# Performance work log

Hardware: AMD Instinct MI355X
Metric: run time of the kernel (lower is better)

## Reference

```python
import jax, jax.numpy as jnp
import numpy as np

H = 2048       # hidden_size
F = 1024       # moe_intermediate_size
E = 32         # n_routed_experts
G = 8          # n_group
TOPK_GROUP = 3
TOP_K = 6      # num_experts_per_tok
N_SHARED = 2
SCALE = 1.0    # routed_scaling_factor
B, S = 1, 2048


def setup_inputs() -> dict:
    key = jax.random.key(0)
    ks = jax.random.split(key, 8)
    std = 0.02
    return {
        "hidden_states": jax.random.normal(ks[0], (B, S, H), dtype=jnp.float32),
        "w_gate": jax.random.normal(ks[1], (E, H), dtype=jnp.float32) * std,
        "wg": jax.random.normal(ks[2], (E, H, F), dtype=jnp.float32) * std,  # stacked gate_proj
        "wu": jax.random.normal(ks[3], (E, H, F), dtype=jnp.float32) * std,  # stacked up_proj
        "wd": jax.random.normal(ks[4], (E, F, H), dtype=jnp.float32) * std,  # stacked down_proj
        "sg": jax.random.normal(ks[5], (N_SHARED * F, H), dtype=jnp.float32) * std,  # shared gate_proj
        "su": jax.random.normal(ks[6], (N_SHARED * F, H), dtype=jnp.float32) * std,  # shared up_proj
        "sd": jax.random.normal(ks[7], (H, N_SHARED * F), dtype=jnp.float32) * std,  # shared down_proj
    }


def reference(hidden_states, w_gate, wg, wu, wd, sg, su, sd):
    b, s, h = hidden_states.shape
    x = hidden_states.reshape(-1, h)                    # [T, H]
    T = x.shape[0]

    # ---- MoEGate (softmax scoring, group_limited_greedy top-k) ----
    logits = x.astype(jnp.float32) @ w_gate.T           # [T, E]
    scores = jax.nn.softmax(logits, axis=-1)
    group_scores = scores.reshape(T, G, E // G).max(axis=-1)          # [T, G]
    _, group_idx = jax.lax.top_k(group_scores, TOPK_GROUP)            # [T, topk_group]
    group_mask = jax.nn.one_hot(group_idx, G, dtype=scores.dtype).sum(axis=1)  # [T, G]
    score_mask = jnp.repeat(group_mask, E // G, axis=-1)              # [T, E]
    tmp_scores = jnp.where(score_mask > 0.5, scores, 0.0)
    topk_weight, topk_idx = jax.lax.top_k(tmp_scores, TOP_K)          # [T, K]
    # norm_topk_prob=True, top_k>1
    topk_weight = topk_weight / (topk_weight.sum(axis=-1, keepdims=True) + 1e-20) * SCALE

    # combine weights per (token, expert): scatter topk weights (indices distinct)
    combine_w = jnp.zeros((T, E), dtype=jnp.float32)
    combine_w = combine_w.at[jnp.arange(T)[:, None], topk_idx].add(topk_weight)

    # ---- routed experts: dense grouped GEMMs, weighted combine ----
    g = jnp.einsum('th,ehf->etf', x, wg)                # [E, T, F]
    u = jnp.einsum('th,ehf->etf', x, wu)                # [E, T, F]
    act = jax.nn.silu(g) * u                            # SiLU gated
    act = act * combine_w.T[:, :, None]                 # fold combine weights before down-proj
    y = jnp.einsum('etf,efh->th', act, wd)              # [T, H]

    # ---- shared experts ----
    shared = (jax.nn.silu(x @ sg.T) * (x @ su.T)) @ sd.T

    return (y + shared).reshape(b, s, h)
```

## Files before the change

### kernel.cpp

```cpp
#include <hip/hip_runtime.h>

#define HD   2048
#define FD   1024
#define NEXP 32
#define TOPK 6
#define TT   2048
#define SDIM 2048
#define NPAIR (TT*TOPK)

typedef __bf16 bf16x8 __attribute__((ext_vector_type(8)));
typedef float  f32x4  __attribute__((ext_vector_type(4)));

#define GLOAD_LDS16(g, l) __builtin_amdgcn_global_load_lds( \
    (const __attribute__((address_space(1))) void*)(g),     \
    (__attribute__((address_space(3))) void*)(l), 16, 0, 0)

#define WAIT_VM4  asm volatile("s_waitcnt vmcnt(4)" ::: "memory")
#define WAIT_VM3  asm volatile("s_waitcnt vmcnt(3)" ::: "memory")
#define WAIT_VM0  asm volatile("s_waitcnt vmcnt(0)" ::: "memory")
#define BAR() do { __builtin_amdgcn_s_barrier(); } while (0)

__device__ __forceinline__ ushort f2b(float f) {
  __bf16 h = (__bf16)f;
  union { __bf16 h; ushort u; } v; v.h = h;
  return v.u;
}

__device__ __forceinline__ int xcd_swz(int bid, int nact) {
  int xcd = bid & 7, i = bid >> 3;
  int q = nact >> 3, r = nact & 7;
  int base = (xcd < r) ? xcd * (q + 1) : r * (q + 1) + (xcd - r) * q;
  return base + i;
}

__device__ __forceinline__ void argmax32(float &v, int &i) {
  #pragma unroll
  for (int m = 16; m >= 1; m >>= 1) {
    float ov = __shfl_xor(v, m, 32);
    int   oi = __shfl_xor(i, m, 32);
    if (ov > v || (ov == v && oi < i)) { v = ov; i = oi; }
  }
}

__global__ __launch_bounds__(64) void gating_kernel(
    const float* __restrict__ x, const float* __restrict__ wgate,
    int* __restrict__ topk_idx, float* __restrict__ topk_w, int* __restrict__ cnt)
{
  int t = blockIdx.x;
  int l = threadIdx.x;
  int e = l & 31;
  int half = l >> 5;
  const float* xr = x + (size_t)t * HD + half * (HD/2);
  const float* wr = wgate + (size_t)e * HD + half * (HD/2);
  float acc = 0.f;
  for (int i = 0; i < HD/2; i += 4) {
    float4 a = *(const float4*)(xr + i);
    float4 b = *(const float4*)(wr + i);
    acc += a.x*b.x + a.y*b.y + a.z*b.z + a.w*b.w;
  }
  acc += __shfl_xor(acc, 32);
  float logit = acc;
  float mx = logit;
  #pragma unroll
  for (int m = 16; m >= 1; m >>= 1) mx = fmaxf(mx, __shfl_xor(mx, m, 32));
  float p = __expf(logit - mx);
  float s = p;
  #pragma unroll
  for (int m = 16; m >= 1; m >>= 1) s += __shfl_xor(s, m, 32);
  float score = p / s;
  float gs = score;
  gs = fmaxf(gs, __shfl_xor(gs, 1, 32));
  gs = fmaxf(gs, __shfl_xor(gs, 2, 32));
  int g = e >> 2;
  float gw = gs;
  bool ingroup = false;
  for (int r = 0; r < 3; ++r) {
    float v = gw; int gi = g;
    argmax32(v, gi);
    if (g == gi) { ingroup = true; gw = -1.f; }
  }
  float ms = ingroup ? score : 0.f;
  int myrank = -1;
  float denom = 1e-20f;
  float mw = ms;
  for (int r = 0; r < 6; ++r) {
    float v = mw; int ei = e;
    argmax32(v, ei);
    denom += v;
    if (e == ei) { myrank = r; mw = -1.f; }
  }
  if (l < 32 && myrank >= 0) {
    topk_idx[t*TOPK + myrank] = e;
    topk_w  [t*TOPK + myrank] = score / denom;
    atomicAdd(&cnt[e], 1);
  }
}

__global__ void scan_kernel(const int* __restrict__ cnt, int* __restrict__ offs,
                            int* __restrict__ tl_e, int* __restrict__ tl_m, int* __restrict__ ntl) {
  if (threadIdx.x == 0) {
    int o = 0, nt = 0;
    for (int e = 0; e < NEXP; ++e) {
      offs[e] = o;
      for (int m = 0; m < cnt[e]; m += 256) { tl_e[nt] = e; tl_m[nt] = m; ++nt; }
      o += cnt[e];
    }
    ntl[0] = nt;
  }
}

__global__ void fill_kernel(const int* __restrict__ topk_idx, const float* __restrict__ topk_w,
                            const int* __restrict__ offs, int* __restrict__ cur,
                            int* __restrict__ pair_tok, float* __restrict__ pair_w)
{
  int idx = blockIdx.x * blockDim.x + threadIdx.x;
  if (idx >= NPAIR) return;
  int e = topk_idx[idx];
  int p = offs[e] + atomicAdd(&cur[e], 1);
  pair_tok[p] = idx / TOPK;
  pair_w[p]   = topk_w[idx];
}

__global__ void cvt_kernel(const float* __restrict__ x, ushort* __restrict__ xb) {
  int i = blockIdx.x * blockDim.x + threadIdx.x;
  float4 v = ((const float4*)x)[i];
  ((ushort4*)xb)[i] = make_ushort4(f2b(v.x), f2b(v.y), f2b(v.z), f2b(v.w));
}

__global__ __launch_bounds__(256) void fconv(const float* __restrict__ in, ushort* __restrict__ out) {
  int i = blockIdx.x * blockDim.x + threadIdx.x;
  float4 v = ((const float4*)in)[i];
  ((ushort4*)out)[i] = make_ushort4(f2b(v.x), f2b(v.y), f2b(v.z), f2b(v.w));
}

#define TSTR 76
__global__ __launch_bounds__(256) void tconv(const float* __restrict__ in, ushort* __restrict__ out,
                                             int R, int C) {
  __shared__ ushort T[64*TSTR];
  int tiles_c = C >> 6;
  int bt = blockIdx.x;
  int r0 = (bt / tiles_c) << 6;
  int c0 = (bt % tiles_c) << 6;
  const float* src = in + (size_t)blockIdx.y * R * C;
  ushort* dst = out + (size_t)blockIdx.y * R * C;
  int t = threadIdx.x;
  int row = (t >> 4) << 2;
  int col4 = (t & 15) << 2;
  float vv[4][4];
  #pragma unroll
  for (int i = 0; i < 4; ++i) {
    float4 v = *(const float4*)(src + (size_t)(r0 + row + i) * C + c0 + col4);
    vv[i][0] = v.x; vv[i][1] = v.y; vv[i][2] = v.z; vv[i][3] = v.w;
  }
  #pragma unroll
  for (int cc = 0; cc < 4; ++cc)
    *(ushort4*)&T[(col4 + cc)*TSTR + row] =
      make_ushort4(f2b(vv[0][cc]), f2b(vv[1][cc]), f2b(vv[2][cc]), f2b(vv[3][cc]));
  __syncthreads();
  #pragma unroll
  for (int p = 0; p < 2; ++p) {
    int item = t + p*256;
    int oc = item >> 3, seg = item & 7;
    ushort4 a = *(const ushort4*)&T[oc*TSTR + seg*8];
    ushort4 b = *(const ushort4*)&T[oc*TSTR + seg*8 + 4];
    ushort* d = dst + (size_t)(c0 + oc) * R + r0 + seg*8;
    *(ushort4*)(d)     = a;
    *(ushort4*)(d + 4) = b;
  }
}


__global__ __launch_bounds__(512, 4) void gu_routed_b(
    const ushort* __restrict__ xb, const ushort* __restrict__ wgt, const ushort* __restrict__ wut,
    const int* __restrict__ pair_tok, const float* __restrict__ pair_w,
    const int* __restrict__ cnt, const int* __restrict__ offs,
    const int* __restrict__ tl_e, const int* __restrict__ tl_m, const int* __restrict__ ntl,
    ushort* __restrict__ act)
{
  __shared__ ushort A[3][256*32];
  __shared__ ushort Bg[3][64*32];
  __shared__ ushort Bu[3][64*32];

  int nact = ntl[0] * 16;
  int bid = blockIdx.x;
  if (bid >= nact) return;
  int wid = xcd_swz(bid, nact);
  int tile = wid >> 4;
  int nt = wid & 15;
  int e  = tl_e[tile];
  int m0 = tl_m[tile];
  int ce = cnt[e];
  int oe = offs[e];
  int n0 = nt * 64;
  int tid = threadIdx.x, lane = tid & 63, w = tid >> 6;

  int csrc = (lane & 3) ^ ((lane >> 3) & 3);
  const ushort* asrc[2];
  #pragma unroll
  for (int j = 0; j < 2; ++j) {
    int r = (2*w + j)*16 + (lane >> 2);
    int pi = min(m0 + r, ce - 1);
    asrc[j] = xb + (size_t)pair_tok[oe + pi] * HD + csrc * 8;
  }
  int tsel = w >> 2;
  int bw = w & 3;
  const ushort* bsrc = (tsel ? wut : wgt) +
      ((size_t)e * FD + n0 + bw*16 + (lane >> 2)) * HD + csrc * 8;
  ushort* bdst0 = tsel ? &Bu[0][bw*512] : &Bg[0][bw*512];
  ushort* bdst1 = tsel ? &Bu[1][bw*512] : &Bg[1][bw*512];
  ushort* bdst2 = tsel ? &Bu[2][bw*512] : &Bg[2][bw*512];

  int lm = lane & 15, lg = lane >> 4;
  int wr = w >> 1, wc = w & 1;
  int asw = (lm >> 1) & 3;

  f32x4 accg[4][2], accu[4][2];
  #pragma unroll
  for (int m = 0; m < 4; ++m)
    #pragma unroll
    for (int n = 0; n < 2; ++n) { accg[m][n] = f32x4{0,0,0,0}; accu[m][n] = f32x4{0,0,0,0}; }

  #define GUB_ISSUE(T, BUF, BD) do { \
    GLOAD_LDS16(asrc[0] + (T)*32, &A[BUF][(2*w)*512]); \
    GLOAD_LDS16(asrc[1] + (T)*32, &A[BUF][(2*w+1)*512]); \
    GLOAD_LDS16(bsrc + (T)*32, BD); \
  } while (0)
  #define GUB_COMPUTE(BUF) do { \
    bf16x8 a[4], bg[2], bu[2]; \
    _Pragma("unroll") \
    for (int m = 0; m < 4; ++m) \
      a[m] = *(const bf16x8*)&A[BUF][(wr*64 + m*16 + lm)*32 + (lg ^ asw)*8]; \
    _Pragma("unroll") \
    for (int n = 0; n < 2; ++n) { \
      int row = wc*32 + n*16 + lm; \
      bg[n] = *(const bf16x8*)&Bg[BUF][row*32 + (lg ^ asw)*8]; \
      bu[n] = *(const bf16x8*)&Bu[BUF][row*32 + (lg ^ asw)*8]; \
    } \
    _Pragma("unroll") \
    for (int m = 0; m < 4; ++m) \
      _Pragma("unroll") \
      for (int n = 0; n < 2; ++n) { \
        accg[m][n] = __builtin_amdgcn_mfma_f32_16x16x32_bf16(a[m], bg[n], accg[m][n], 0, 0, 0); \
        accu[m][n] = __builtin_amdgcn_mfma_f32_16x16x32_bf16(a[m], bu[n], accu[m][n], 0, 0, 0); \
      } \
  } while (0)

  GUB_ISSUE(0, 0, bdst0);
  GUB_ISSUE(1, 1, bdst1);
  WAIT_VM3;
  BAR();

  for (int tt = 0; tt < 20; ++tt) {
    int t = tt * 3;
    GUB_ISSUE(t+2, 2, bdst2); GUB_COMPUTE(0); WAIT_VM3; BAR();
    GUB_ISSUE(t+3, 0, bdst0); GUB_COMPUTE(1); WAIT_VM3; BAR();
    GUB_ISSUE(t+4, 1, bdst1); GUB_COMPUTE(2); WAIT_VM3; BAR();
  }
  GUB_ISSUE(62, 2, bdst2); GUB_COMPUTE(0); WAIT_VM3; BAR();
  GUB_ISSUE(63, 0, bdst0); GUB_COMPUTE(1); WAIT_VM3; BAR();
  GUB_COMPUTE(2); WAIT_VM0; BAR();
  GUB_COMPUTE(0);
  #undef GUB_ISSUE
  #undef GUB_COMPUTE

  #pragma unroll
  for (int m = 0; m < 4; ++m) {
    #pragma unroll
    for (int j = 0; j < 4; ++j) {
      int rl = wr*64 + m*16 + lg*4 + j;
      int pi = m0 + rl;
      if (pi >= ce) continue;
      float pwv = pair_w[oe + pi];
      size_t base = (size_t)(oe + pi) * FD + n0 + wc*32;
      #pragma unroll
      for (int n = 0; n < 2; ++n) {
        float gv = accg[m][n][j];
        float uv = accu[m][n][j];
        float sv = gv / (1.f + __expf(-gv));
        act[base + n*16 + lm] = f2b(sv * uv * pwv);
      }
    }
  }
}

__global__ __launch_bounds__(512, 4) void down_routed_b(
    const ushort* __restrict__ act, const ushort* __restrict__ wdt,
    const int* __restrict__ pair_tok, const int* __restrict__ cnt, const int* __restrict__ offs,
    const int* __restrict__ tl_e, const int* __restrict__ tl_m, const int* __restrict__ ntl,
    float* __restrict__ y)
{
  __shared__ ushort A[3][256*32];
  __shared__ ushort Bd[3][128*32];

  int nact = ntl[0] * 16;
  int bid = blockIdx.x;
  if (bid >= nact) return;
  int wid = xcd_swz(bid, nact);
  int tile = wid >> 4;
  int nt = wid & 15;
  int e  = tl_e[tile];
  int m0 = tl_m[tile];
  int ce = cnt[e];
  int oe = offs[e];
  int n0 = nt * 128;
  int tid = threadIdx.x, lane = tid & 63, w = tid >> 6;

  int csrc = (lane & 3) ^ ((lane >> 3) & 3);
  const ushort* asrc[2];
  #pragma unroll
  for (int j = 0; j < 2; ++j) {
    int r = (2*w + j)*16 + (lane >> 2);
    int pi = min(m0 + r, ce - 1);
    asrc[j] = act + (size_t)(oe + pi) * FD + csrc * 8;
  }
  const ushort* bsrc = wdt + ((size_t)e * HD + n0 + w*16 + (lane >> 2)) * FD + csrc * 8;

  int lm = lane & 15, lg = lane >> 4;
  int wr = w >> 1, wc = w & 1;
  int asw = (lm >> 1) & 3;

  f32x4 acc[4][4];
  #pragma unroll
  for (int m = 0; m < 4; ++m)
    #pragma unroll
    for (int n = 0; n < 4; ++n) acc[m][n] = f32x4{0,0,0,0};

  #define DNB_ISSUE(T, BUF) do { \
    GLOAD_LDS16(asrc[0] + (T)*32, &A[BUF][(2*w)*512]); \
    GLOAD_LDS16(asrc[1] + (T)*32, &A[BUF][(2*w+1)*512]); \
    GLOAD_LDS16(bsrc + (T)*32, &Bd[BUF][w*512]); \
  } while (0)
  #define DNB_COMPUTE(BUF) do { \
    bf16x8 a[4], b[4]; \
    _Pragma("unroll") \
    for (int m = 0; m < 4; ++m) \
      a[m] = *(const bf16x8*)&A[BUF][(wr*64 + m*16 + lm)*32 + (lg ^ asw)*8]; \
    _Pragma("unroll") \
    for (int n = 0; n < 4; ++n) { \
      int row = wc*64 + n*16 + lm; \
      b[n] = *(const bf16x8*)&Bd[BUF][row*32 + (lg ^ asw)*8]; \
    } \
    _Pragma("unroll") \
    for (int m = 0; m < 4; ++m) \
      _Pragma("unroll") \
      for (int n = 0; n < 4; ++n) \
        acc[m][n] = __builtin_amdgcn_mfma_f32_16x16x32_bf16(a[m], b[n], acc[m][n], 0, 0, 0); \
  } while (0)

  DNB_ISSUE(0, 0);
  DNB_ISSUE(1, 1);
  WAIT_VM3;
  BAR();

  for (int tt = 0; tt < 10; ++tt) {
    int t = tt * 3;
    DNB_ISSUE(t+2, 2); DNB_COMPUTE(0); WAIT_VM3; BAR();
    DNB_ISSUE(t+3, 0); DNB_COMPUTE(1); WAIT_VM3; BAR();
    DNB_ISSUE(t+4, 1); DNB_COMPUTE(2); WAIT_VM3; BAR();
  }
  DNB_COMPUTE(0); WAIT_VM0; BAR();
  DNB_COMPUTE(1);
  #undef DNB_ISSUE
  #undef DNB_COMPUTE

  #pragma unroll
  for (int m = 0; m < 4; ++m) {
    #pragma unroll
    for (int j = 0; j < 4; ++j) {
      int rl = wr*64 + m*16 + lg*4 + j;
      int pi = m0 + rl;
      if (pi >= ce) continue;
      int tok = pair_tok[oe + pi];
      size_t base = (size_t)tok * HD + n0 + wc*64;
      #pragma unroll
      for (int n = 0; n < 4; ++n)
        atomicAdd(&y[base + n*16 + lm], acc[m][n][j]);
    }
  }
}

__global__ __launch_bounds__(256) void shared_gu_b(
    const ushort* __restrict__ xb, const ushort* __restrict__ sgb, const ushort* __restrict__ sub,
    ushort* __restrict__ sact)
{
  __shared__ ushort A[3][128*32];
  __shared__ ushort Bg[3][64*32];
  __shared__ ushort Bu[3][64*32];

  int bid = blockIdx.x;
  int wid = (bid & 7) * 64 + (bid >> 3);
  int mt = wid & 15;
  int nt = wid >> 4;
  int m0 = mt * 128;
  int n0 = nt * 64;
  int tid = threadIdx.x, lane = tid & 63, w = tid >> 6;

  int csrc = (lane & 3) ^ ((lane >> 3) & 3);
  const ushort* asrc[2];
  #pragma unroll
  for (int j = 0; j < 2; ++j) {
    int r = (2*w + j)*16 + (lane >> 2);
    asrc[j] = xb + (size_t)(m0 + r) * HD + csrc * 8;
  }
  int brow = w*16 + (lane >> 2);
  const ushort* bgsrc = sgb + (size_t)(n0 + brow) * HD + csrc * 8;
  const ushort* busrc = sub + (size_t)(n0 + brow) * HD + csrc * 8;

  int lm = lane & 15, lg = lane >> 4;
  int wr = w >> 1, wc = w & 1;
  int asw = (lm >> 1) & 3;

  f32x4 accg[4][2], accu[4][2];
  #pragma unroll
  for (int m = 0; m < 4; ++m)
    #pragma unroll
    for (int n = 0; n < 2; ++n) { accg[m][n] = f32x4{0,0,0,0}; accu[m][n] = f32x4{0,0,0,0}; }

  #define SGB_ISSUE(T, BUF) do { \
    GLOAD_LDS16(asrc[0] + (T)*32, &A[BUF][(2*w)*512]); \
    GLOAD_LDS16(asrc[1] + (T)*32, &A[BUF][(2*w+1)*512]); \
    GLOAD_LDS16(bgsrc + (T)*32, &Bg[BUF][w*512]); \
    GLOAD_LDS16(busrc + (T)*32, &Bu[BUF][w*512]); \
  } while (0)
  #define SGB_COMPUTE(BUF) do { \
    bf16x8 a[4], bg[2], bu[2]; \
    _Pragma("unroll") \
    for (int m = 0; m < 4; ++m) \
      a[m] = *(const bf16x8*)&A[BUF][(wr*64 + m*16 + lm)*32 + (lg ^ asw)*8]; \
    _Pragma("unroll") \
    for (int n = 0; n < 2; ++n) { \
      int row = wc*32 + n*16 + lm; \
      bg[n] = *(const bf16x8*)&Bg[BUF][row*32 + (lg ^ asw)*8]; \
      bu[n] = *(const bf16x8*)&Bu[BUF][row*32 + (lg ^ asw)*8]; \
    } \
    _Pragma("unroll") \
    for (int m = 0; m < 4; ++m) \
      _Pragma("unroll") \
      for (int n = 0; n < 2; ++n) { \
        accg[m][n] = __builtin_amdgcn_mfma_f32_16x16x32_bf16(a[m], bg[n], accg[m][n], 0, 0, 0); \
        accu[m][n] = __builtin_amdgcn_mfma_f32_16x16x32_bf16(a[m], bu[n], accu[m][n], 0, 0, 0); \
      } \
  } while (0)

  SGB_ISSUE(0, 0);
  SGB_ISSUE(1, 1);
  WAIT_VM4;
  BAR();

  for (int tt = 0; tt < 20; ++tt) {
    int t = tt * 3;
    SGB_ISSUE(t+2, 2); SGB_COMPUTE(0); WAIT_VM4; BAR();
    SGB_ISSUE(t+3, 0); SGB_COMPUTE(1); WAIT_VM4; BAR();
    SGB_ISSUE(t+4, 1); SGB_COMPUTE(2); WAIT_VM4; BAR();
  }
  SGB_ISSUE(62, 2); SGB_COMPUTE(0); WAIT_VM4; BAR();
  SGB_ISSUE(63, 0); SGB_COMPUTE(1); WAIT_VM4; BAR();
  SGB_COMPUTE(2); WAIT_VM0; BAR();
  SGB_COMPUTE(0);
  #undef SGB_ISSUE
  #undef SGB_COMPUTE

  #pragma unroll
  for (int m = 0; m < 4; ++m) {
    #pragma unroll
    for (int j = 0; j < 4; ++j) {
      int rl = wr*64 + m*16 + lg*4 + j;
      size_t base = (size_t)(m0 + rl) * SDIM + n0 + wc*32;
      #pragma unroll
      for (int n = 0; n < 2; ++n) {
        float gv = accg[m][n][j];
        float uv = accu[m][n][j];
        float sv = gv / (1.f + __expf(-gv));
        sact[base + n*16 + lm] = f2b(sv * uv);
      }
    }
  }
}

__global__ __launch_bounds__(256) void shared_down_b(
    const ushort* __restrict__ sact, const ushort* __restrict__ sdb, float* __restrict__ y)
{
  __shared__ ushort A[3][128*32];
  __shared__ ushort Bd[3][128*32];

  int bid = blockIdx.x;
  int wid = (bid & 7) * 32 + (bid >> 3);
  int mt = wid & 15;
  int nt = wid >> 4;
  int m0 = mt * 128;
  int n0 = nt * 128;
  int tid = threadIdx.x, lane = tid & 63, w = tid >> 6;

  int csrc = (lane & 3) ^ ((lane >> 3) & 3);
  const ushort* asrc[2];
  const ushort* bsrc[2];
  #pragma unroll
  for (int j = 0; j < 2; ++j) {
    int r = (2*w + j)*16 + (lane >> 2);
    asrc[j] = sact + (size_t)(m0 + r) * SDIM + csrc * 8;
    bsrc[j] = sdb + (size_t)(n0 + r) * SDIM + csrc * 8;
  }

  int lm = lane & 15, lg = lane >> 4;
  int wr = w >> 1, wc = w & 1;
  int asw = (lm >> 1) & 3;

  f32x4 acc[4][4];
  #pragma unroll
  for (int m = 0; m < 4; ++m)
    #pragma unroll
    for (int n = 0; n < 4; ++n) acc[m][n] = f32x4{0,0,0,0};

  #define SDB_ISSUE(T, BUF) do { \
    GLOAD_LDS16(asrc[0] + (T)*32, &A[BUF][(2*w)*512]); \
    GLOAD_LDS16(asrc[1] + (T)*32, &A[BUF][(2*w+1)*512]); \
    GLOAD_LDS16(bsrc[0] + (T)*32, &Bd[BUF][(2*w)*512]); \
    GLOAD_LDS16(bsrc[1] + (T)*32, &Bd[BUF][(2*w+1)*512]); \
  } while (0)
  #define SDB_COMPUTE(BUF) do { \
    bf16x8 a[4], b[4]; \
    _Pragma("unroll") \
    for (int m = 0; m < 4; ++m) \
      a[m] = *(const bf16x8*)&A[BUF][(wr*64 + m*16 + lm)*32 + (lg ^ asw)*8]; \
    _Pragma("unroll") \
    for (int n = 0; n < 4; ++n) { \
      int row = wc*64 + n*16 + lm; \
      b[n] = *(const bf16x8*)&Bd[BUF][row*32 + (lg ^ asw)*8]; \
    } \
    _Pragma("unroll") \
    for (int m = 0; m < 4; ++m) \
      _Pragma("unroll") \
      for (int n = 0; n < 4; ++n) \
        acc[m][n] = __builtin_amdgcn_mfma_f32_16x16x32_bf16(a[m], b[n], acc[m][n], 0, 0, 0); \
  } while (0)

  SDB_ISSUE(0, 0);
  SDB_ISSUE(1, 1);
  WAIT_VM4;
  BAR();

  for (int tt = 0; tt < 20; ++tt) {
    int t = tt * 3;
    SDB_ISSUE(t+2, 2); SDB_COMPUTE(0); WAIT_VM4; BAR();
    SDB_ISSUE(t+3, 0); SDB_COMPUTE(1); WAIT_VM4; BAR();
    SDB_ISSUE(t+4, 1); SDB_COMPUTE(2); WAIT_VM4; BAR();
  }
  SDB_ISSUE(62, 2); SDB_COMPUTE(0); WAIT_VM4; BAR();
  SDB_ISSUE(63, 0); SDB_COMPUTE(1); WAIT_VM4; BAR();
  SDB_COMPUTE(2); WAIT_VM0; BAR();
  SDB_COMPUTE(0);
  #undef SDB_ISSUE
  #undef SDB_COMPUTE

  #pragma unroll
  for (int m = 0; m < 4; ++m) {
    #pragma unroll
    for (int j = 0; j < 4; ++j) {
      int rl = wr*64 + m*16 + lg*4 + j;
      size_t base = (size_t)(m0 + rl) * HD + n0 + wc*64;
      #pragma unroll
      for (int n = 0; n < 4; ++n)
        y[base + n*16 + lm] = acc[m][n][j];
    }
  }
}

extern "C" void kernel_launch(void* const* d_in, const int* in_sizes, int n_in,
                              void* d_out, int out_size, void* d_ws, size_t ws_size,
                              hipStream_t stream) {
  const float* x     = (const float*)d_in[0];
  const float* wgate = (const float*)d_in[1];
  const float* wg    = (const float*)d_in[2];
  const float* wu    = (const float*)d_in[3];
  const float* wd    = (const float*)d_in[4];
  const float* sg    = (const float*)d_in[5];
  const float* su    = (const float*)d_in[6];
  const float* sd    = (const float*)d_in[7];
  float* y = (float*)d_out;
  char* ws = (char*)d_ws;

  ushort* xb   = (ushort*)(ws + 0);
  ushort* act  = (ushort*)(ws + 8388608);
  ushort* sact = (ushort*)(ws + 33554432);
  int*    tidx = (int*)  (ws + 41943040);
  float*  tw   = (float*)(ws + 41992192);
  int*    ptok = (int*)  (ws + 42041344);
  float*  pw   = (float*)(ws + 42090496);
  int*    cnt  = (int*)  (ws + 42139648);
  int*    curc = (int*)  (ws + 42139776);
  int*    offs = (int*)  (ws + 42139904);
  int*    tl_e = (int*)  (ws + 42140160);
  int*    tl_m = (int*)  (ws + 42140672);
  int*    ntl  = (int*)  (ws + 42141184);
  ushort* wgt  = (ushort*)(ws + 50331648);
  ushort* wut  = (ushort*)(ws + 184549376);
  ushort* wdt  = (ushort*)(ws + 318767104);
  ushort* sgb  = (ushort*)(ws + 452984832);
  ushort* sub  = (ushort*)(ws + 461373440);
  ushort* sdb  = (ushort*)(ws + 469762048);

  hipMemsetAsync(cnt, 0, 512, stream);

  cvt_kernel<<<dim3(4096), dim3(256), 0, stream>>>(x, xb);
  gating_kernel<<<dim3(TT), dim3(64), 0, stream>>>(x, wgate, tidx, tw, cnt);
  scan_kernel<<<dim3(1), dim3(64), 0, stream>>>(cnt, offs, tl_e, tl_m, ntl);
  fill_kernel<<<dim3(48), dim3(256), 0, stream>>>(tidx, tw, offs, curc, ptok, pw);

  tconv<<<dim3(512, NEXP), dim3(256), 0, stream>>>(wg, wgt, HD, FD);
  tconv<<<dim3(512, NEXP), dim3(256), 0, stream>>>(wu, wut, HD, FD);
  tconv<<<dim3(512, NEXP), dim3(256), 0, stream>>>(wd, wdt, FD, HD);
  fconv<<<dim3(4096), dim3(256), 0, stream>>>(sg, sgb);
  fconv<<<dim3(4096), dim3(256), 0, stream>>>(su, sub);
  fconv<<<dim3(4096), dim3(256), 0, stream>>>(sd, sdb);

  shared_gu_b<<<dim3(512), dim3(256), 0, stream>>>(xb, sgb, sub, sact);
  shared_down_b<<<dim3(256), dim3(256), 0, stream>>>(sact, sdb, y);
  gu_routed_b<<<dim3(1280), dim3(512), 0, stream>>>(xb, wgt, wut, ptok, pw, cnt, offs,
                                                    tl_e, tl_m, ntl, act);
  down_routed_b<<<dim3(1280), dim3(512), 0, stream>>>(act, wdt, ptok, cnt, offs,
                                                      tl_e, tl_m, ntl, y);
}
```

Before: 753.3 us.

## Replace routed down-proj atomics with per-pair bf16 output and gather combine; enlarge shared-expert tiles

The routed down-projection now writes each (token, expert) pair's result as bf16 into a pair-ordered buffer instead of doing float atomicAdds into y. A new combine kernel gathers the six pair rows per token through an inverse index built in fill_kernel and adds them to y. The shared-expert kernels move to 512-thread blocks with 256-row M tiles and fewer B-loads per thread. This removes atomic contention but adds a separate combine pass and rounds the pair partial sums to bf16, which could affect accuracy. The pair buffer reuses the transposed gate-weight workspace, which is safe only because gu_routed_b has already finished reading it.

```diff
diff --git a/kernel.cpp b/kernel.cpp
--- a/kernel.cpp
+++ b/kernel.cpp
@@ -15,7 +15,6 @@
     (const __attribute__((address_space(1))) void*)(g),     \
     (__attribute__((address_space(3))) void*)(l), 16, 0, 0)
 
-#define WAIT_VM4  asm volatile("s_waitcnt vmcnt(4)" ::: "memory")
 #define WAIT_VM3  asm volatile("s_waitcnt vmcnt(3)" ::: "memory")
 #define WAIT_VM0  asm volatile("s_waitcnt vmcnt(0)" ::: "memory")
 #define BAR() do { __builtin_amdgcn_s_barrier(); } while (0)
@@ -24,6 +23,10 @@
   __bf16 h = (__bf16)f;
   union { __bf16 h; ushort u; } v; v.h = h;
   return v.u;
+}
+__device__ __forceinline__ float b2f(ushort u) {
+  union { unsigned u; float f; } v; v.u = (unsigned)u << 16;
+  return v.f;
 }
 
 __device__ __forceinline__ int xcd_swz(int bid, int nact) {
@@ -111,7 +114,8 @@
 
 __global__ void fill_kernel(const int* __restrict__ topk_idx, const float* __restrict__ topk_w,
                             const int* __restrict__ offs, int* __restrict__ cur,
-                            int* __restrict__ pair_tok, float* __restrict__ pair_w)
+                            int* __restrict__ pair_tok, float* __restrict__ pair_w,
+                            int* __restrict__ inv)
 {
   int idx = blockIdx.x * blockDim.x + threadIdx.x;
   if (idx >= NPAIR) return;
@@ -119,6 +123,7 @@
   int p = offs[e] + atomicAdd(&cur[e], 1);
   pair_tok[p] = idx / TOPK;
   pair_w[p]   = topk_w[idx];
+  inv[idx]    = p;
 }
 
 __global__ void cvt_kernel(const float* __restrict__ x, ushort* __restrict__ xb) {
@@ -169,6 +174,29 @@
   }
 }
 
+__global__ __launch_bounds__(256) void combine_kernel(
+    const ushort* __restrict__ pairout, const int* __restrict__ inv, float* __restrict__ y)
+{
+  int t = blockIdx.x;
+  int h0 = threadIdx.x * 8;
+  const int* iv = inv + t*TOPK;
+  float* yr = y + (size_t)t * HD + h0;
+  float4 y0 = *(const float4*)(yr);
+  float4 y1 = *(const float4*)(yr + 4);
+  float acc[8] = {y0.x, y0.y, y0.z, y0.w, y1.x, y1.y, y1.z, y1.w};
+  #pragma unroll
+  for (int r = 0; r < TOPK; ++r) {
+    int p = iv[r];
+    const ushort* pr = pairout + (size_t)p * HD + h0;
+    ushort4 a = *(const ushort4*)(pr);
+    ushort4 b = *(const ushort4*)(pr + 4);
+    acc[0] += b2f(a.x); acc[1] += b2f(a.y); acc[2] += b2f(a.z); acc[3] += b2f(a.w);
+    acc[4] += b2f(b.x); acc[5] += b2f(b.y); acc[6] += b2f(b.z); acc[7] += b2f(b.w);
+  }
+  *(float4*)(yr)     = make_float4(acc[0], acc[1], acc[2], acc[3]);
+  *(float4*)(yr + 4) = make_float4(acc[4], acc[5], acc[6], acc[7]);
+}
+
 
 __global__ __launch_bounds__(512, 4) void gu_routed_b(
     const ushort* __restrict__ xb, const ushort* __restrict__ wgt, const ushort* __restrict__ wut,
@@ -285,9 +313,9 @@
 
 __global__ __launch_bounds__(512, 4) void down_routed_b(
     const ushort* __restrict__ act, const ushort* __restrict__ wdt,
-    const int* __restrict__ pair_tok, const int* __restrict__ cnt, const int* __restrict__ offs,
+    const int* __restrict__ cnt, const int* __restrict__ offs,
     const int* __restrict__ tl_e, const int* __restrict__ tl_m, const int* __restrict__ ntl,
-    float* __restrict__ y)
+    ushort* __restrict__ pairout)
 {
   __shared__ ushort A[3][256*32];
   __shared__ ushort Bd[3][128*32];
@@ -370,28 +398,27 @@
       int rl = wr*64 + m*16 + lg*4 + j;
       int pi = m0 + rl;
       if (pi >= ce) continue;
-      int tok = pair_tok[oe + pi];
-      size_t base = (size_t)tok * HD + n0 + wc*64;
+      size_t base = (size_t)(oe + pi) * HD + n0 + wc*64;
       #pragma unroll
       for (int n = 0; n < 4; ++n)
-        atomicAdd(&y[base + n*16 + lm], acc[m][n][j]);
+        pairout[base + n*16 + lm] = f2b(acc[m][n][j]);
     }
   }
 }
 
-__global__ __launch_bounds__(256) void shared_gu_b(
+__global__ __launch_bounds__(512, 4) void shared_gu_b(
     const ushort* __restrict__ xb, const ushort* __restrict__ sgb, const ushort* __restrict__ sub,
     ushort* __restrict__ sact)
 {
-  __shared__ ushort A[3][128*32];
+  __shared__ ushort A[3][256*32];
   __shared__ ushort Bg[3][64*32];
   __shared__ ushort Bu[3][64*32];
 
   int bid = blockIdx.x;
-  int wid = (bid & 7) * 64 + (bid >> 3);
-  int mt = wid & 15;
-  int nt = wid >> 4;
-  int m0 = mt * 128;
+  int wid = (bid & 7) * 32 + (bid >> 3);
+  int mt = wid & 7;
+  int nt = wid >> 3;
+  int m0 = mt * 256;
   int n0 = nt * 64;
   int tid = threadIdx.x, lane = tid & 63, w = tid >> 6;
 
@@ -402,9 +429,12 @@
     int r = (2*w + j)*16 + (lane >> 2);
     asrc[j] = xb + (size_t)(m0 + r) * HD + csrc * 8;
   }
-  int brow = w*16 + (lane >> 2);
-  const ushort* bgsrc = sgb + (size_t)(n0 + brow) * HD + csrc * 8;
-  const ushort* busrc = sub + (size_t)(n0 + brow) * HD + csrc * 8;
+  int tsel = w >> 2;
+  int bw = w & 3;
+  const ushort* bsrc = (tsel ? sub : sgb) + (size_t)(n0 + bw*16 + (lane >> 2)) * HD + csrc * 8;
+  ushort* bdst0 = tsel ? &Bu[0][bw*512] : &Bg[0][bw*512];
+  ushort* bdst1 = tsel ? &Bu[1][bw*512] : &Bg[1][bw*512];
+  ushort* bdst2 = tsel ? &Bu[2][bw*512] : &Bg[2][bw*512];
 
   int lm = lane & 15, lg = lane >> 4;
   int wr = w >> 1, wc = w & 1;
@@ -416,11 +446,10 @@
     #pragma unroll
     for (int n = 0; n < 2; ++n) { accg[m][n] = f32x4{0,0,0,0}; accu[m][n] = f32x4{0,0,0,0}; }
 
-  #define SGB_ISSUE(T, BUF) do { \
+  #define SGB_ISSUE(T, BUF, BD) do { \
     GLOAD_LDS16(asrc[0] + (T)*32, &A[BUF][(2*w)*512]); \
     GLOAD_LDS16(asrc[1] + (T)*32, &A[BUF][(2*w+1)*512]); \
-    GLOAD_LDS16(bgsrc + (T)*32, &Bg[BUF][w*512]); \
-    GLOAD_LDS16(busrc + (T)*32, &Bu[BUF][w*512]); \
+    GLOAD_LDS16(bsrc + (T)*32, BD); \
   } while (0)
   #define SGB_COMPUTE(BUF) do { \
     bf16x8 a[4], bg[2], bu[2]; \
@@ -442,19 +471,19 @@
       } \
   } while (0)
 
-  SGB_ISSUE(0, 0);
-  SGB_ISSUE(1, 1);
-  WAIT_VM4;
+  SGB_ISSUE(0, 0, bdst0);
+  SGB_ISSUE(1, 1, bdst1);
+  WAIT_VM3;
   BAR();
 
   for (int tt = 0; tt < 20; ++tt) {
     int t = tt * 3;
-    SGB_ISSUE(t+2, 2); SGB_COMPUTE(0); WAIT_VM4; BAR();
-    SGB_ISSUE(t+3, 0); SGB_COMPUTE(1); WAIT_VM4; BAR();
-    SGB_ISSUE(t+4, 1); SGB_COMPUTE(2); WAIT_VM4; BAR();
-  }
-  SGB_ISSUE(62, 2); SGB_COMPUTE(0); WAIT_VM4; BAR();
-  SGB_ISSUE(63, 0); SGB_COMPUTE(1); WAIT_VM4; BAR();
+    SGB_ISSUE(t+2, 2, bdst2); SGB_COMPUTE(0); WAIT_VM3; BAR();
+    SGB_ISSUE(t+3, 0, bdst0); SGB_COMPUTE(1); WAIT_VM3; BAR();
+    SGB_ISSUE(t+4, 1, bdst1); SGB_COMPUTE(2); WAIT_VM3; BAR();
+  }
+  SGB_ISSUE(62, 2, bdst2); SGB_COMPUTE(0); WAIT_VM3; BAR();
+  SGB_ISSUE(63, 0, bdst0); SGB_COMPUTE(1); WAIT_VM3; BAR();
   SGB_COMPUTE(2); WAIT_VM0; BAR();
   SGB_COMPUTE(0);
   #undef SGB_ISSUE
@@ -477,29 +506,28 @@
   }
 }
 
-__global__ __launch_bounds__(256) void shared_down_b(
+__global__ __launch_bounds__(512, 4) void shared_down_b(
     const ushort* __restrict__ sact, const ushort* __restrict__ sdb, float* __restrict__ y)
 {
-  __shared__ ushort A[3][128*32];
+  __shared__ ushort A[3][256*32];
   __shared__ ushort Bd[3][128*32];
 
   int bid = blockIdx.x;
-  int wid = (bid & 7) * 32 + (bid >> 3);
-  int mt = wid & 15;
-  int nt = wid >> 4;
-  int m0 = mt * 128;
+  int wid = (bid & 7) * 16 + (bid >> 3);
+  int mt = wid & 7;
+  int nt = wid >> 3;
+  int m0 = mt * 256;
   int n0 = nt * 128;
   int tid = threadIdx.x, lane = tid & 63, w = tid >> 6;
 
   int csrc = (lane & 3) ^ ((lane >> 3) & 3);
   const ushort* asrc[2];
-  const ushort* bsrc[2];
   #pragma unroll
   for (int j = 0; j < 2; ++j) {
     int r = (2*w + j)*16 + (lane >> 2);
     asrc[j] = sact + (size_t)(m0 + r) * SDIM + csrc * 8;
-    bsrc[j] = sdb + (size_t)(n0 + r) * SDIM + csrc * 8;
-  }
+  }
+  const ushort* bsrc = sdb + (size_t)(n0 + w*16 + (lane >> 2)) * SDIM + csrc * 8;
 
   int lm = lane & 15, lg = lane >> 4;
   int wr = w >> 1, wc = w & 1;
@@ -514,8 +542,7 @@
   #define SDB_ISSUE(T, BUF) do { \
     GLOAD_LDS16(asrc[0] + (T)*32, &A[BUF][(2*w)*512]); \
     GLOAD_LDS16(asrc[1] + (T)*32, &A[BUF][(2*w+1)*512]); \
-    GLOAD_LDS16(bsrc[0] + (T)*32, &Bd[BUF][(2*w)*512]); \
-    GLOAD_LDS16(bsrc[1] + (T)*32, &Bd[BUF][(2*w+1)*512]); \
+    GLOAD_LDS16(bsrc + (T)*32, &Bd[BUF][w*512]); \
   } while (0)
   #define SDB_COMPUTE(BUF) do { \
     bf16x8 a[4], b[4]; \
@@ -536,17 +563,17 @@
 
   SDB_ISSUE(0, 0);
   SDB_ISSUE(1, 1);
-  WAIT_VM4;
+  WAIT_VM3;
   BAR();
 
   for (int tt = 0; tt < 20; ++tt) {
     int t = tt * 3;
-    SDB_ISSUE(t+2, 2); SDB_COMPUTE(0); WAIT_VM4; BAR();
-    SDB_ISSUE(t+3, 0); SDB_COMPUTE(1); WAIT_VM4; BAR();
-    SDB_ISSUE(t+4, 1); SDB_COMPUTE(2); WAIT_VM4; BAR();
-  }
-  SDB_ISSUE(62, 2); SDB_COMPUTE(0); WAIT_VM4; BAR();
-  SDB_ISSUE(63, 0); SDB_COMPUTE(1); WAIT_VM4; BAR();
+    SDB_ISSUE(t+2, 2); SDB_COMPUTE(0); WAIT_VM3; BAR();
+    SDB_ISSUE(t+3, 0); SDB_COMPUTE(1); WAIT_VM3; BAR();
+    SDB_ISSUE(t+4, 1); SDB_COMPUTE(2); WAIT_VM3; BAR();
+  }
+  SDB_ISSUE(62, 2); SDB_COMPUTE(0); WAIT_VM3; BAR();
+  SDB_ISSUE(63, 0); SDB_COMPUTE(1); WAIT_VM3; BAR();
   SDB_COMPUTE(2); WAIT_VM0; BAR();
   SDB_COMPUTE(0);
   #undef SDB_ISSUE
@@ -592,19 +619,21 @@
   int*    tl_e = (int*)  (ws + 42140160);
   int*    tl_m = (int*)  (ws + 42140672);
   int*    ntl  = (int*)  (ws + 42141184);
+  int*    inv  = (int*)  (ws + 42141440);
   ushort* wgt  = (ushort*)(ws + 50331648);
   ushort* wut  = (ushort*)(ws + 184549376);
   ushort* wdt  = (ushort*)(ws + 318767104);
   ushort* sgb  = (ushort*)(ws + 452984832);
   ushort* sub  = (ushort*)(ws + 461373440);
   ushort* sdb  = (ushort*)(ws + 469762048);
+  ushort* pairout = wgt;
 
   hipMemsetAsync(cnt, 0, 512, stream);
 
   cvt_kernel<<<dim3(4096), dim3(256), 0, stream>>>(x, xb);
   gating_kernel<<<dim3(TT), dim3(64), 0, stream>>>(x, wgate, tidx, tw, cnt);
   scan_kernel<<<dim3(1), dim3(64), 0, stream>>>(cnt, offs, tl_e, tl_m, ntl);
-  fill_kernel<<<dim3(48), dim3(256), 0, stream>>>(tidx, tw, offs, curc, ptok, pw);
+  fill_kernel<<<dim3(48), dim3(256), 0, stream>>>(tidx, tw, offs, curc, ptok, pw, inv);
 
   tconv<<<dim3(512, NEXP), dim3(256), 0, stream>>>(wg, wgt, HD, FD);
   tconv<<<dim3(512, NEXP), dim3(256), 0, stream>>>(wu, wut, HD, FD);
@@ -613,10 +642,11 @@
   fconv<<<dim3(4096), dim3(256), 0, stream>>>(su, sub);
   fconv<<<dim3(4096), dim3(256), 0, stream>>>(sd, sdb);
 
-  shared_gu_b<<<dim3(512), dim3(256), 0, stream>>>(xb, sgb, sub, sact);
-  shared_down_b<<<dim3(256), dim3(256), 0, stream>>>(sact, sdb, y);
+  shared_gu_b<<<dim3(256), dim3(512), 0, stream>>>(xb, sgb, sub, sact);
+  shared_down_b<<<dim3(128), dim3(512), 0, stream>>>(sact, sdb, y);
   gu_routed_b<<<dim3(1280), dim3(512), 0, stream>>>(xb, wgt, wut, ptok, pw, cnt, offs,
                                                     tl_e, tl_m, ntl, act);
-  down_routed_b<<<dim3(1280), dim3(512), 0, stream>>>(act, wdt, ptok, cnt, offs,
-                                                      tl_e, tl_m, ntl, y);
-}
+  down_routed_b<<<dim3(1280), dim3(512), 0, stream>>>(act, wdt, cnt, offs,
+                                                      tl_e, tl_m, ntl, pairout);
+  combine_kernel<<<dim3(TT), dim3(256), 0, stream>>>(pairout, inv, y);
+}
```

New measurement: 727.8 us. 3.4% less time.
